# Performance work log

Measured on AMD Instinct MI355X. Metric: run time of the kernel, lower is better.

## Reference

```python
import jax, jax.numpy as jnp
import numpy as np

BLOCK = 32      # block_size
KB = 128        # K // BLOCK (mask rows)
NB = 128        # N // BLOCK (mask cols)
DENSITY = 0.1


def _make_mask_indices():
    rng = np.random.RandomState(0)
    mask = rng.rand(KB, NB) < DENSITY
    # guarantee no fully-empty output column (kernel writes zeros there anyway,
    # segment_sum also yields zeros, so this is only to keep stats sane)
    ii, jj = np.nonzero(mask)   # row-major order == torch.nonzero(mask)
    return ii.astype(np.int32), jj.astype(np.int32)


def setup_inputs() -> dict:
    key = jax.random.key(0)
    k1, k2 = jax.random.split(key)
    ii, jj = _make_mask_indices()
    nnz = ii.shape[0]
    M = 4096
    K = KB * BLOCK
    x = jax.random.normal(k1, (M, K), dtype=jnp.float32)
    # block-sparse weight: one [BLOCK, BLOCK] tile per nonzero mask entry,
    # stored in row-major nonzero order (matches torch.nonzero ordering)
    w = jax.random.normal(k2, (nnz, BLOCK, BLOCK), dtype=jnp.float32) * 0.02
    return {"x": x, "w": w, "idx_i": jnp.asarray(ii), "idx_j": jnp.asarray(jj)}


def reference(x, w, idx_i, idx_j):
    # y[:, j*B:(j+1)*B] += x[:, i*B:(i+1)*B] @ w[blk] for each nonzero block (i, j)
    M, K = x.shape
    nnz, B, _ = w.shape
    xb = x.reshape(M, K // B, B)[:, idx_i, :]                 # [M, nnz, B] gather
    partial = jnp.einsum('mnk,nkj->nmj', xb, w)               # [nnz, M, B]
    yb = jax.ops.segment_sum(partial, idx_j, num_segments=NB)  # [NB, M, B] scatter-add
    return yb.transpose(1, 0, 2).reshape(M, NB * B)           # [M, N]
```

## Files before the change

### kernel.cpp

```cpp
#include <hip/hip_runtime.h>
#include <hip/hip_bf16.h>

typedef __bf16 bf16x8 __attribute__((ext_vector_type(8)));
typedef __bf16 bf16x4 __attribute__((ext_vector_type(4)));
typedef float f32x4 __attribute__((ext_vector_type(4)));

#define KDIM 4096
#define NDIM 4096
#define NBJ  128

__global__ __launch_bounds__(256) void k_cvt_x(const float* __restrict__ x,
                                               __bf16* __restrict__ xb) {
    int i = blockIdx.x * 256 + threadIdx.x;
    float4 u = ((const float4*)x)[2 * i];
    float4 v = ((const float4*)x)[2 * i + 1];
    bf16x8 o;
    o[0] = (__bf16)u.x; o[1] = (__bf16)u.y; o[2] = (__bf16)u.z; o[3] = (__bf16)u.w;
    o[4] = (__bf16)v.x; o[5] = (__bf16)v.y; o[6] = (__bf16)v.z; o[7] = (__bf16)v.w;
    ((bf16x8*)xb)[i] = o;
}

__global__ __launch_bounds__(256) void k_wtrans(const float* __restrict__ w,
                                                __bf16* __restrict__ wT) {
    __shared__ __bf16 tile[32][33];
    int n = blockIdx.x, t = threadIdx.x;
    float4 v = ((const float4*)(w + (size_t)n * 1024))[t];
    int e = t * 4, k = e >> 5, c = e & 31;
    tile[k][c + 0] = (__bf16)v.x; tile[k][c + 1] = (__bf16)v.y;
    tile[k][c + 2] = (__bf16)v.z; tile[k][c + 3] = (__bf16)v.w;
    __syncthreads();
    int f = t * 4, cc = f >> 5, kk = f & 31;
    bf16x4 o;
    o[0] = tile[kk + 0][cc]; o[1] = tile[kk + 1][cc];
    o[2] = tile[kk + 2][cc]; o[3] = tile[kk + 3][cc];
    ((bf16x4*)(wT + (size_t)n * 1024))[t] = o;
}

__global__ __launch_bounds__(256) void k_csc(const int* __restrict__ idx_j,
                                             int* __restrict__ colptr,
                                             int* __restrict__ collist, int nnz) {
    __shared__ int cnt[NBJ];
    int t = threadIdx.x;
    for (int i = t; i < NBJ; i += 256) cnt[i] = 0;
    __syncthreads();
    for (int n = t; n < nnz; n += 256) atomicAdd(&cnt[idx_j[n]], 1);
    __syncthreads();
    if (t == 0) {
        int run = 0;
        for (int j = 0; j < NBJ; ++j) { int c = cnt[j]; colptr[j] = run; cnt[j] = run; run += c; }
        colptr[NBJ] = run;
    }
    __syncthreads();
    for (int n = t; n < nnz; n += 256) {
        int j = idx_j[n];
        int pos = atomicAdd(&cnt[j], 1);
        collist[pos] = n;
    }
}

__global__ __launch_bounds__(256) void k_bsmm(
    const __bf16* __restrict__ x, const __bf16* __restrict__ wT,
    const int* __restrict__ colptr, const int* __restrict__ collist,
    const int* __restrict__ idx_i, float* __restrict__ y) {
    int j    = blockIdx.y;
    int lane = threadIdx.x & 63, wave = threadIdx.x >> 6;
    int quad = lane >> 4, l16 = lane & 15;
    int wrow = blockIdx.x * 256 + wave * 64;

    f32x4 acc[4][2] = {};

    int beg = colptr[j], end = colptr[j + 1];
    for (int p = beg; p < end; ++p) {
        int n  = collist[p];
        int ib = idx_i[n];
        const __bf16* xp = x + (size_t)(wrow + l16) * KDIM + ib * 32 + quad * 8;
        bf16x8 a0 = *(const bf16x8*)(xp);
        bf16x8 a1 = *(const bf16x8*)(xp + 16 * KDIM);
        bf16x8 a2 = *(const bf16x8*)(xp + 32 * KDIM);
        bf16x8 a3 = *(const bf16x8*)(xp + 48 * KDIM);
        const __bf16* wp = wT + (size_t)n * 1024 + l16 * 32 + quad * 8;
        bf16x8 b0 = *(const bf16x8*)(wp);
        bf16x8 b1 = *(const bf16x8*)(wp + 512);
        acc[0][0] = __builtin_amdgcn_mfma_f32_16x16x32_bf16(a0, b0, acc[0][0], 0, 0, 0);
        acc[0][1] = __builtin_amdgcn_mfma_f32_16x16x32_bf16(a0, b1, acc[0][1], 0, 0, 0);
        acc[1][0] = __builtin_amdgcn_mfma_f32_16x16x32_bf16(a1, b0, acc[1][0], 0, 0, 0);
        acc[1][1] = __builtin_amdgcn_mfma_f32_16x16x32_bf16(a1, b1, acc[1][1], 0, 0, 0);
        acc[2][0] = __builtin_amdgcn_mfma_f32_16x16x32_bf16(a2, b0, acc[2][0], 0, 0, 0);
        acc[2][1] = __builtin_amdgcn_mfma_f32_16x16x32_bf16(a2, b1, acc[2][1], 0, 0, 0);
        acc[3][0] = __builtin_amdgcn_mfma_f32_16x16x32_bf16(a3, b0, acc[3][0], 0, 0, 0);
        acc[3][1] = __builtin_amdgcn_mfma_f32_16x16x32_bf16(a3, b1, acc[3][1], 0, 0, 0);
    }

    #pragma unroll
    for (int r = 0; r < 4; ++r)
        #pragma unroll
        for (int ch = 0; ch < 2; ++ch)
            #pragma unroll
            for (int reg = 0; reg < 4; ++reg) {
                int row = wrow + r * 16 + quad * 4 + reg;
                int col = j * 32 + ch * 16 + l16;
                y[(size_t)row * NDIM + col] = acc[r][ch][reg];
            }
}

__global__ __launch_bounds__(256) void k_bsmm_nows(
    const float* __restrict__ x, const float* __restrict__ w,
    const int* __restrict__ idx_i, const int* __restrict__ idx_j,
    float* __restrict__ y, int nnz) {
    __shared__ int list[256];
    __shared__ int listn;
    __shared__ __bf16 tw[32][40];
    int j    = blockIdx.y;
    int tid  = threadIdx.x;
    int lane = tid & 63;
    int wave = tid >> 6;
    int quad = lane >> 4, l16 = lane & 15;
    int wrow = blockIdx.x * 256 + wave * 64;

    if (tid == 0) listn = 0;
    __syncthreads();
    for (int n = tid; n < nnz; n += 256)
        if (idx_j[n] == j) { int p = atomicAdd(&listn, 1); list[p & 255] = n; }
    __syncthreads();
    int cnt = listn;

    f32x4 acc[4][2] = {};
    for (int p = 0; p < cnt; ++p) {
        int n  = list[p];
        int ib = idx_i[n];
        {
            float4 v = ((const float4*)(w + (size_t)n * 1024))[tid];
            int e = tid * 4, k = e >> 5, c = e & 31;
            tw[c + 0][k] = (__bf16)v.x; tw[c + 1][k] = (__bf16)v.y;
            tw[c + 2][k] = (__bf16)v.z; tw[c + 3][k] = (__bf16)v.w;
        }
        __syncthreads();
        bf16x8 a[4];
        #pragma unroll
        for (int r = 0; r < 4; ++r) {
            const float* xp = x + (size_t)(wrow + r * 16 + l16) * KDIM + ib * 32 + quad * 8;
            float4 u = *(const float4*)(xp);
            float4 v = *(const float4*)(xp + 4);
            a[r][0] = (__bf16)u.x; a[r][1] = (__bf16)u.y; a[r][2] = (__bf16)u.z; a[r][3] = (__bf16)u.w;
            a[r][4] = (__bf16)v.x; a[r][5] = (__bf16)v.y; a[r][6] = (__bf16)v.z; a[r][7] = (__bf16)v.w;
        }
        bf16x8 b0 = *(const bf16x8*)&tw[l16][quad * 8];
        bf16x8 b1 = *(const bf16x8*)&tw[l16 + 16][quad * 8];
        #pragma unroll
        for (int r = 0; r < 4; ++r) {
            acc[r][0] = __builtin_amdgcn_mfma_f32_16x16x32_bf16(a[r], b0, acc[r][0], 0, 0, 0);
            acc[r][1] = __builtin_amdgcn_mfma_f32_16x16x32_bf16(a[r], b1, acc[r][1], 0, 0, 0);
        }
        __syncthreads();
    }

    #pragma unroll
    for (int r = 0; r < 4; ++r)
        #pragma unroll
        for (int ch = 0; ch < 2; ++ch)
            #pragma unroll
            for (int reg = 0; reg < 4; ++reg) {
                int row = wrow + r * 16 + quad * 4 + reg;
                int col = j * 32 + ch * 16 + l16;
                y[(size_t)row * NDIM + col] = acc[r][ch][reg];
            }
}

extern "C" void kernel_launch(void* const* d_in, const int* in_sizes, int n_in,
                              void* d_out, int out_size, void* d_ws, size_t ws_size,
                              hipStream_t stream) {
    const float* x     = (const float*)d_in[0];
    const float* w     = (const float*)d_in[1];
    const int*   idx_i = (const int*)d_in[2];
    const int*   idx_j = (const int*)d_in[3];
    float*       y     = (float*)d_out;

    int nnz = in_sizes[2];
    int M   = in_sizes[0] / KDIM;
    dim3 grid(M / 256, NBJ);

    size_t xb_bytes = (size_t)M * KDIM * 2;
    size_t wt_bytes = (size_t)nnz * 1024 * 2;
    size_t need = xb_bytes + wt_bytes + (size_t)(NBJ + 1 + 3) * 4 + (size_t)nnz * 4;

    if (ws_size >= need) {
        __bf16* xb      = (__bf16*)d_ws;
        __bf16* wT      = (__bf16*)((char*)d_ws + xb_bytes);
        int*    colptr  = (int*)((char*)d_ws + xb_bytes + wt_bytes);
        int*    collist = colptr + NBJ + 1 + 3;
        int nx = (M * KDIM) / 8 / 256;
        k_cvt_x<<<nx, 256, 0, stream>>>(x, xb);
        k_wtrans<<<nnz, 256, 0, stream>>>(w, wT);
        k_csc<<<1, 256, 0, stream>>>(idx_j, colptr, collist, nnz);
        k_bsmm<<<grid, 256, 0, stream>>>(xb, wT, colptr, collist, idx_i, y);
    } else {
        k_bsmm_nows<<<grid, 256, 0, stream>>>(x, w, idx_i, idx_j, y, nnz);
    }
}
```

Measured before the change: 200.7 us.

## Block-major bf16 x layout, packed column info, prefetched fragments in bsmm

Converts x into a block-column-major bf16 layout ([KB][M][32]) so each 32-wide K block is contiguous per row chunk. The CSC build now uses a parallel prefix scan and packs idx_i together with the nonzero index into a single int, which is broadcast via lane shuffles. The bsmm loop double-buffers fragment loads, fetching the next block while the current MFMAs run. A remapped 1D grid interleaves columns across workgroups for locality. The packing limits nnz to 16 bits, and register use rises because of the prefetch.

```diff
diff --git a/kernel.cpp b/kernel.cpp
--- a/kernel.cpp
+++ b/kernel.cpp
@@ -8,16 +8,20 @@
 #define KDIM 4096
 #define NDIM 4096
 #define NBJ  128
+#define KB   128
 
 __global__ __launch_bounds__(256) void k_cvt_x(const float* __restrict__ x,
-                                               __bf16* __restrict__ xb) {
-    int i = blockIdx.x * 256 + threadIdx.x;
-    float4 u = ((const float4*)x)[2 * i];
-    float4 v = ((const float4*)x)[2 * i + 1];
+                                               __bf16* __restrict__ xb, int M) {
+    int i  = blockIdx.x;
+    int m0 = blockIdx.y * 64;
+    int q  = threadIdx.x & 3, r = threadIdx.x >> 2;
+    const float* xp = x + (size_t)(m0 + r) * KDIM + i * 32 + q * 8;
+    float4 u = ((const float4*)xp)[0];
+    float4 v = ((const float4*)xp)[1];
     bf16x8 o;
-    o[0] = (__bf16)u.x; o[1] = (__bf16)u.y; o[2] = (__bf16)u.z; o[3] = (__bf16)u.w;
-    o[4] = (__bf16)v.x; o[5] = (__bf16)v.y; o[6] = (__bf16)v.z; o[7] = (__bf16)v.w;
-    ((bf16x8*)xb)[i] = o;
+    o[0]=(__bf16)u.x; o[1]=(__bf16)u.y; o[2]=(__bf16)u.z; o[3]=(__bf16)u.w;
+    o[4]=(__bf16)v.x; o[5]=(__bf16)v.y; o[6]=(__bf16)v.z; o[7]=(__bf16)v.w;
+    *(bf16x8*)(xb + ((size_t)i * M + m0 + r) * 32 + q * 8) = o;
 }
 
 __global__ __launch_bounds__(256) void k_wtrans(const float* __restrict__ w,
@@ -36,59 +40,88 @@
     ((bf16x4*)(wT + (size_t)n * 1024))[t] = o;
 }
 
-__global__ __launch_bounds__(256) void k_csc(const int* __restrict__ idx_j,
+__global__ __launch_bounds__(256) void k_csc(const int* __restrict__ idx_i,
+                                             const int* __restrict__ idx_j,
                                              int* __restrict__ colptr,
-                                             int* __restrict__ collist, int nnz) {
-    __shared__ int cnt[NBJ];
+                                             int* __restrict__ colinfo, int nnz) {
+    __shared__ int cnt[NBJ], cur[NBJ];
     int t = threadIdx.x;
-    for (int i = t; i < NBJ; i += 256) cnt[i] = 0;
+    if (t < NBJ) cnt[t] = 0;
     __syncthreads();
     for (int n = t; n < nnz; n += 256) atomicAdd(&cnt[idx_j[n]], 1);
     __syncthreads();
-    if (t == 0) {
-        int run = 0;
-        for (int j = 0; j < NBJ; ++j) { int c = cnt[j]; colptr[j] = run; cnt[j] = run; run += c; }
-        colptr[NBJ] = run;
+    int mycount = (t < NBJ) ? cnt[t] : 0;
+    for (int off = 1; off < NBJ; off <<= 1) {
+        int add = (t < NBJ && t >= off) ? cnt[t - off] : 0;
+        __syncthreads();
+        if (t < NBJ) cnt[t] += add;
+        __syncthreads();
+    }
+    if (t < NBJ) {
+        colptr[t + 1] = cnt[t];
+        cur[t] = cnt[t] - mycount;
+        if (t == 0) colptr[0] = 0;
     }
     __syncthreads();
     for (int n = t; n < nnz; n += 256) {
         int j = idx_j[n];
-        int pos = atomicAdd(&cnt[j], 1);
-        collist[pos] = n;
-    }
-}
+        int pos = atomicAdd(&cur[j], 1);
+        colinfo[pos] = (idx_i[n] << 16) | n;
+    }
+}
+
+struct Frag { bf16x8 a0, a1, a2, a3, b0, b1; };
 
 __global__ __launch_bounds__(256) void k_bsmm(
-    const __bf16* __restrict__ x, const __bf16* __restrict__ wT,
-    const int* __restrict__ colptr, const int* __restrict__ collist,
-    const int* __restrict__ idx_i, float* __restrict__ y) {
-    int j    = blockIdx.y;
+    const __bf16* __restrict__ xb, const __bf16* __restrict__ wT,
+    const int* __restrict__ colptr, const int* __restrict__ colinfo,
+    float* __restrict__ y, int M) {
+    int RCH = M >> 8;
+    int l = blockIdx.x;
+    int s = l & 7, t = l >> 3;
+    int j = (t / RCH) * 8 + s;
+    int rc = t % RCH;
     int lane = threadIdx.x & 63, wave = threadIdx.x >> 6;
     int quad = lane >> 4, l16 = lane & 15;
-    int wrow = blockIdx.x * 256 + wave * 64;
+    int wrow = rc * 256 + wave * 64;
+
+    int beg = colptr[j], end = colptr[j + 1];
+    int cnt = end - beg;
 
     f32x4 acc[4][2] = {};
 
-    int beg = colptr[j], end = colptr[j + 1];
-    for (int p = beg; p < end; ++p) {
-        int n  = collist[p];
-        int ib = idx_i[n];
-        const __bf16* xp = x + (size_t)(wrow + l16) * KDIM + ib * 32 + quad * 8;
-        bf16x8 a0 = *(const bf16x8*)(xp);
-        bf16x8 a1 = *(const bf16x8*)(xp + 16 * KDIM);
-        bf16x8 a2 = *(const bf16x8*)(xp + 32 * KDIM);
-        bf16x8 a3 = *(const bf16x8*)(xp + 48 * KDIM);
-        const __bf16* wp = wT + (size_t)n * 1024 + l16 * 32 + quad * 8;
-        bf16x8 b0 = *(const bf16x8*)(wp);
-        bf16x8 b1 = *(const bf16x8*)(wp + 512);
-        acc[0][0] = __builtin_amdgcn_mfma_f32_16x16x32_bf16(a0, b0, acc[0][0], 0, 0, 0);
-        acc[0][1] = __builtin_amdgcn_mfma_f32_16x16x32_bf16(a0, b1, acc[0][1], 0, 0, 0);
-        acc[1][0] = __builtin_amdgcn_mfma_f32_16x16x32_bf16(a1, b0, acc[1][0], 0, 0, 0);
-        acc[1][1] = __builtin_amdgcn_mfma_f32_16x16x32_bf16(a1, b1, acc[1][1], 0, 0, 0);
-        acc[2][0] = __builtin_amdgcn_mfma_f32_16x16x32_bf16(a2, b0, acc[2][0], 0, 0, 0);
-        acc[2][1] = __builtin_amdgcn_mfma_f32_16x16x32_bf16(a2, b1, acc[2][1], 0, 0, 0);
-        acc[3][0] = __builtin_amdgcn_mfma_f32_16x16x32_bf16(a3, b0, acc[3][0], 0, 0, 0);
-        acc[3][1] = __builtin_amdgcn_mfma_f32_16x16x32_bf16(a3, b1, acc[3][1], 0, 0, 0);
+    if (cnt > 0) {
+        int einfo = colinfo[beg + (lane < cnt ? lane : cnt - 1)];
+
+        auto fetch = [&](int p) {
+            int ee = (p < 64) ? __shfl(einfo, p) : colinfo[beg + p];
+            int n = ee & 0xFFFF, ib = ee >> 16;
+            Frag f;
+            const __bf16* xp = xb + ((size_t)ib * M + wrow + l16) * 32 + quad * 8;
+            f.a0 = *(const bf16x8*)(xp);
+            f.a1 = *(const bf16x8*)(xp + 16 * 32);
+            f.a2 = *(const bf16x8*)(xp + 32 * 32);
+            f.a3 = *(const bf16x8*)(xp + 48 * 32);
+            const __bf16* wp = wT + (size_t)n * 1024 + l16 * 32 + quad * 8;
+            f.b0 = *(const bf16x8*)(wp);
+            f.b1 = *(const bf16x8*)(wp + 512);
+            return f;
+        };
+
+        Frag c = fetch(0);
+        for (int p = 0; p < cnt; ++p) {
+            Frag nx = c;
+            if (p + 1 < cnt) nx = fetch(p + 1);
+            acc[0][0] = __builtin_amdgcn_mfma_f32_16x16x32_bf16(c.a0, c.b0, acc[0][0], 0, 0, 0);
+            acc[0][1] = __builtin_amdgcn_mfma_f32_16x16x32_bf16(c.a0, c.b1, acc[0][1], 0, 0, 0);
+            acc[1][0] = __builtin_amdgcn_mfma_f32_16x16x32_bf16(c.a1, c.b0, acc[1][0], 0, 0, 0);
+            acc[1][1] = __builtin_amdgcn_mfma_f32_16x16x32_bf16(c.a1, c.b1, acc[1][1], 0, 0, 0);
+            acc[2][0] = __builtin_amdgcn_mfma_f32_16x16x32_bf16(c.a2, c.b0, acc[2][0], 0, 0, 0);
+            acc[2][1] = __builtin_amdgcn_mfma_f32_16x16x32_bf16(c.a2, c.b1, acc[2][1], 0, 0, 0);
+            acc[3][0] = __builtin_amdgcn_mfma_f32_16x16x32_bf16(c.a3, c.b0, acc[3][0], 0, 0, 0);
+            acc[3][1] = __builtin_amdgcn_mfma_f32_16x16x32_bf16(c.a3, c.b1, acc[3][1], 0, 0, 0);
+            c = nx;
+        }
     }
 
     #pragma unroll
@@ -110,10 +143,9 @@
     __shared__ int list[256];
     __shared__ int listn;
     __shared__ __bf16 tw[32][40];
-    int j    = blockIdx.y;
-    int tid  = threadIdx.x;
-    int lane = tid & 63;
-    int wave = tid >> 6;
+    int j = blockIdx.y;
+    int tid = threadIdx.x;
+    int lane = tid & 63, wave = tid >> 6;
     int quad = lane >> 4, l16 = lane & 15;
     int wrow = blockIdx.x * 256 + wave * 64;
 
@@ -126,7 +158,7 @@
 
     f32x4 acc[4][2] = {};
     for (int p = 0; p < cnt; ++p) {
-        int n  = list[p];
+        int n = list[p];
         int ib = idx_i[n];
         {
             float4 v = ((const float4*)(w + (size_t)n * 1024))[tid];
@@ -177,23 +209,21 @@
 
     int nnz = in_sizes[2];
     int M   = in_sizes[0] / KDIM;
-    dim3 grid(M / 256, NBJ);
 
     size_t xb_bytes = (size_t)M * KDIM * 2;
     size_t wt_bytes = (size_t)nnz * 1024 * 2;
-    size_t need = xb_bytes + wt_bytes + (size_t)(NBJ + 1 + 3) * 4 + (size_t)nnz * 4;
-
-    if (ws_size >= need) {
+    size_t need = xb_bytes + wt_bytes + (size_t)(NBJ + 2 + nnz) * 4;
+
+    if (ws_size >= need && (M & 255) == 0) {
         __bf16* xb      = (__bf16*)d_ws;
         __bf16* wT      = (__bf16*)((char*)d_ws + xb_bytes);
         int*    colptr  = (int*)((char*)d_ws + xb_bytes + wt_bytes);
-        int*    collist = colptr + NBJ + 1 + 3;
-        int nx = (M * KDIM) / 8 / 256;
-        k_cvt_x<<<nx, 256, 0, stream>>>(x, xb);
+        int*    colinfo = colptr + NBJ + 1;
+        k_cvt_x<<<dim3(KB, M / 64), 256, 0, stream>>>(x, xb, M);
         k_wtrans<<<nnz, 256, 0, stream>>>(w, wT);
-        k_csc<<<1, 256, 0, stream>>>(idx_j, colptr, collist, nnz);
-        k_bsmm<<<grid, 256, 0, stream>>>(xb, wT, colptr, collist, idx_i, y);
+        k_csc<<<1, 256, 0, stream>>>(idx_i, idx_j, colptr, colinfo, nnz);
+        k_bsmm<<<(M / 256) * NBJ, 256, 0, stream>>>(xb, wT, colptr, colinfo, y, M);
     } else {
-        k_bsmm_nows<<<grid, 256, 0, stream>>>(x, w, idx_i, idx_j, y, nnz);
-    }
-}
+        k_bsmm_nows<<<dim3(M / 256, NBJ), 256, 0, stream>>>(x, w, idx_i, idx_j, y, nnz);
+    }
+}
```

Result: no change. 197.4 us (-1.7%).
